# Optimization experiments

Hardware: AMD Instinct MI355X
Metric: run time of the kernel (lower is better)

Reference implementation:

```python
import jax, jax.numpy as jnp
import numpy as np

N, E, IN, HID, H, OUT, G = 20000, 320000, 128, 64, 6, 10, 64
NEG_SLOPE = 0.2


def gat_conv(x, W, a_src, a_dst, b, src, dst):
    # x: [N, F_in]; W: [F_in, H*C]; a_src/a_dst: [H, C]; b: [H*C]
    n = x.shape[0]
    h = (x @ W).reshape(n, H, HID)                      # [N, H, C]
    alpha_s = jnp.einsum('nhc,hc->nh', h, a_src)        # [N, H]
    alpha_d = jnp.einsum('nhc,hc->nh', h, a_dst)
    e = jax.nn.leaky_relu(alpha_s[src] + alpha_d[dst], NEG_SLOPE)  # [E, H]
    # segment softmax over incoming edges of each destination node
    m = jax.ops.segment_max(e, dst, num_segments=n)
    ex = jnp.exp(e - m[dst])
    s = jax.ops.segment_sum(ex, dst, num_segments=n)
    alpha = ex / (s[dst] + 1e-16)                       # [E, H]
    out = jax.ops.segment_sum(alpha[:, :, None] * h[src], dst, num_segments=n)
    return out.reshape(n, H * HID) + b


def setup_inputs() -> dict:
    key = jax.random.key(0)
    ks = jax.random.split(key, 24)
    p = lambda k, shp: jax.random.normal(k, shp, dtype=jnp.float32) * 0.1
    inp = {
        'x': jax.random.normal(ks[0], (N, IN), dtype=jnp.float32),
        'edge_index': jax.random.randint(ks[1], (2, E), 0, N),
        'batch': jnp.sort(jax.random.randint(ks[2], (N,), 0, G)),
        'W1': p(ks[3], (IN, H * HID)), 'a1_src': p(ks[4], (H, HID)), 'a1_dst': p(ks[5], (H, HID)), 'b1': p(ks[6], (H * HID,)),
        'W2': p(ks[7], (H * HID, H * HID)), 'a2_src': p(ks[8], (H, HID)), 'a2_dst': p(ks[9], (H, HID)), 'b2': p(ks[10], (H * HID,)),
        'Ws1': p(ks[11], (IN, H * HID)), 'as1_src': p(ks[12], (H, HID)), 'as1_dst': p(ks[13], (H, HID)), 'bs1': p(ks[14], (H * HID,)),
        'Ws2': p(ks[15], (H * HID, H * HID)), 'as2_src': p(ks[16], (H, HID)), 'as2_dst': p(ks[17], (H, HID)), 'bs2': p(ks[18], (H * HID,)),
        'r1_w': p(ks[19], (H * HID, HID)), 'r1_b': p(ks[20], (HID,)),
        'r2_w': p(ks[21], (HID, OUT)), 'r2_b': p(ks[22], (OUT,)),
    }
    return inp


def reference(x, edge_index, batch, W1, a1_src, a1_dst, b1, W2, a2_src, a2_dst, b2,
              Ws1, as1_src, as1_dst, bs1, Ws2, as2_src, as2_dst, bs2,
              r1_w, r1_b, r2_w, r2_b):
    # PyG GATConv adds self-loops by default
    loop = jnp.arange(N, dtype=edge_index.dtype)
    src = jnp.concatenate([edge_index[0], loop])
    dst = jnp.concatenate([edge_index[1], loop])

    # skip branch (dropout = identity in eval)
    xs = jax.nn.relu(gat_conv(x, Ws1, as1_src, as1_dst, bs1, src, dst))
    xs = jax.nn.relu(gat_conv(xs, Ws2, as2_src, as2_dst, bs2, src, dst))

    # main branch
    h = jax.nn.relu(gat_conv(x, W1, a1_src, a1_dst, b1, src, dst))
    h = jax.nn.relu(gat_conv(h, W2, a2_src, a2_dst, b2, src, dst))

    h = h + xs

    # global mean pool over graphs
    sums = jax.ops.segment_sum(h, batch, num_segments=G)          # [G, H*C]
    cnts = jax.ops.segment_sum(jnp.ones((N,), h.dtype), batch, num_segments=G)
    x_readout = sums / jnp.maximum(cnts, 1.0)[:, None]

    x_global = jax.nn.relu(x_readout @ r1_w + r1_b) @ r2_w + r2_b  # [G, OUT]
    return (jnp.squeeze(x_global), x_readout)
```

## Files before the change

### kernel.cpp

```cpp
#include <hip/hip_runtime.h>
#include <hip/hip_fp16.h>

#define NN 20000
#define EE 320000
#define ETOT 340000
#define FIN 128
#define NH 6
#define FF 384
#define NOUT 10
#define NG 64
#define NEG 0.2f
#define PCH 32
#define NB ((NN + 255) / 256)

typedef short short8 __attribute__((ext_vector_type(8)));
typedef float f32x4 __attribute__((ext_vector_type(4)));

__device__ __half g_h16[(size_t)NN * FF];
__device__ float g_bufB[(size_t)NN * FF];
__device__ float g_bufC[(size_t)NN * FF];
__device__ unsigned short g_featHi[(size_t)NN * FF];
__device__ unsigned short g_xHi[(size_t)NN * FIN];
__device__ unsigned short g_WtHi[4][FF * FF];
__device__ float g_alS[4][NN * NH];
__device__ float g_alD[4][NN * NH];
__device__ int g_rowptr[NN + 1];
__device__ int g_cnt[NN];
__device__ int g_cur[NN];
__device__ int g_blocksum[NB];
__device__ int g_colsrc[ETOT];
__device__ float g_pool[NG * FF];
__device__ int g_gcnt[NG];

__device__ __forceinline__ unsigned short f2bf(float f) {
  unsigned u = __float_as_uint(f);
  u += 0x7FFFu + ((u >> 16) & 1u);
  return (unsigned short)(u >> 16);
}
__device__ __forceinline__ float bf2f(unsigned short s) {
  return __uint_as_float(((unsigned)s) << 16);
}

__device__ __forceinline__ void gl_lds16(const void* g, void* l) {
  __builtin_amdgcn_global_load_lds(
      (const __attribute__((address_space(1))) unsigned int*)(unsigned long long)g,
      (__attribute__((address_space(3))) unsigned int*)(unsigned int)(unsigned long long)l,
      16, 0, 0);
}

__device__ __forceinline__ void mfma_acc(f32x4& c, short8 a, short8 b) {
  asm("v_mfma_f32_16x16x32_bf16 %0, %1, %2, %0" : "+v"(c) : "v"(a), "v"(b));
}

__device__ __forceinline__ void fmix(float2& acc, unsigned hv, float w) {
  asm("v_fma_mix_f32 %0, %2, %3, %0 op_sel:[0,0,0] op_sel_hi:[1,0,0]\n\t"
      "v_fma_mix_f32 %1, %2, %3, %1 op_sel:[1,0,0] op_sel_hi:[1,0,0]"
      : "+v"(acc.x), "+v"(acc.y)
      : "v"(hv), "v"(w));
}

__global__ __launch_bounds__(256) void k_wprep(const float* __restrict__ W, int K, int widx) {
  int i = blockIdx.x * 256 + threadIdx.x;
  if (i >= K * FF) return;
  int k = i / FF, c = i % FF;
  g_WtHi[widx][c * K + k] = f2bf(W[i]);
}

__global__ __launch_bounds__(256) void k_zero() {
  int i = blockIdx.x * 256 + threadIdx.x;
  if (i < NN) g_cnt[i] = 0;
  if (i < NG * FF) g_pool[i] = 0.f;
  if (i < NG) g_gcnt[i] = 0;
  if (i < 4 * NN * NH) {
    (&g_alS[0][0])[i] = 0.f;
    (&g_alD[0][0])[i] = 0.f;
  }
}

__global__ __launch_bounds__(256) void k_hist(const int* __restrict__ ei) {
  int i = blockIdx.x * 256 + threadIdx.x;
  if (i >= ETOT) return;
  int d = (i < EE) ? ei[EE + i] : (i - EE);
  atomicAdd(&g_cnt[d], 1);
}

__global__ __launch_bounds__(256) void k_scan_blk() {
  int b = blockIdx.x;
  int tid = threadIdx.x;
  int i = b * 256 + tid;
  int lane = tid & 63, wid = tid >> 6;
  int v = (i < NN) ? g_cnt[i] : 0;
  int s = v;
  #pragma unroll
  for (int off = 1; off < 64; off <<= 1) {
    int t = __shfl_up(s, off);
    if (lane >= off) s += t;
  }
  __shared__ int wsum[4];
  if (lane == 63) wsum[wid] = s;
  __syncthreads();
  int woff = 0;
  #pragma unroll
  for (int w = 0; w < 4; ++w) woff += (w < wid) ? wsum[w] : 0;
  if (i < NN) g_rowptr[i] = woff + s - v;
  if (tid == 0) g_blocksum[b] = wsum[0] + wsum[1] + wsum[2] + wsum[3];
}

__global__ __launch_bounds__(128) void k_scan_top() {
  int tid = threadIdx.x;
  int lane = tid & 63, wid = tid >> 6;
  int v = (tid < NB) ? g_blocksum[tid] : 0;
  int s = v;
  #pragma unroll
  for (int off = 1; off < 64; off <<= 1) {
    int t = __shfl_up(s, off);
    if (lane >= off) s += t;
  }
  __shared__ int wsum[2];
  if (lane == 63) wsum[wid] = s;
  __syncthreads();
  int woff = (wid == 1) ? wsum[0] : 0;
  int excl = woff + s - v;
  if (tid < NB) g_blocksum[tid] = excl;
  if (tid == NB - 1) g_rowptr[NN] = excl + v;
}

__global__ __launch_bounds__(256) void k_scan_add() {
  int i = blockIdx.x * 256 + threadIdx.x;
  if (i >= NN) return;
  int r = g_rowptr[i] + g_blocksum[blockIdx.x];
  g_rowptr[i] = r;
  g_cur[i] = r;
}

__global__ __launch_bounds__(256) void k_scatter(const int* __restrict__ ei) {
  int i = blockIdx.x * 256 + threadIdx.x;
  if (i >= ETOT) return;
  int s, d;
  if (i < EE) { s = ei[i]; d = ei[EE + i]; } else { s = d = i - EE; }
  int pos = atomicAdd(&g_cur[d], 1);
  g_colsrc[pos] = s;
}

__global__ __launch_bounds__(256) void k_split(const float* __restrict__ xin) {
  int n4 = (NN * FIN) >> 2;
  const float4* s4 = (const float4*)xin;
  ushort4* oh4 = (ushort4*)g_xHi;
  for (int i = blockIdx.x * blockDim.x + threadIdx.x; i < n4; i += gridDim.x * blockDim.x) {
    float4 v = s4[i];
    ushort4 h;
    h.x = f2bf(v.x);
    h.y = f2bf(v.y);
    h.z = f2bf(v.z);
    h.w = f2bf(v.w);
    oh4[i] = h;
  }
}

__global__ __launch_bounds__(256) void k_gemm(int asel, int widx, int K, int layer,
                                              const float* __restrict__ asr,
                                              const float* __restrict__ adt) {
  __shared__ unsigned short lA[128 * 64];
  __shared__ unsigned short lB[128 * 64];
  const unsigned short* Ah = asel ? g_featHi : g_xHi;
  const unsigned short* Bh = g_WtHi[widx];
  const int m0 = blockIdx.x * 128;
  const int n0 = blockIdx.y * 128;
  const int tid = threadIdx.x;
  const int wave = tid >> 6, lane = tid & 63;
  const int wm = wave >> 1, wn = wave & 1;
  const int srow = lane >> 3;
  const int scol = (lane & 7) * 8;

  f32x4 acc[4][4] = {};

  for (int k0 = 0; k0 < K; k0 += 64) {
    __syncthreads();
    #pragma unroll
    for (int it = 0; it < 4; ++it) {
      int c = wave * 4 + it;
      int rA = c * 8 + srow;
      int gr = m0 + rA; gr = (gr < NN) ? gr : (NN - 1);
      gl_lds16(Ah + (size_t)gr * K + k0 + scol, (unsigned short*)lA + c * 512);
      int cB = n0 + rA;
      gl_lds16(Bh + (size_t)cB * K + k0 + scol, (unsigned short*)lB + c * 512);
    }
    __syncthreads();
    #pragma unroll
    for (int kk = 0; kk < 64; kk += 32) {
      const int kb = kk + (lane >> 4) * 8;
      const int r16 = lane & 15;
      short8 af[4], bfr[4];
      #pragma unroll
      for (int mf = 0; mf < 4; ++mf)
        af[mf] = *(const short8*)&lA[(wm * 64 + mf * 16 + r16) * 64 + kb];
      #pragma unroll
      for (int nf = 0; nf < 4; ++nf)
        bfr[nf] = *(const short8*)&lB[(wn * 64 + nf * 16 + r16) * 64 + kb];
      #pragma unroll
      for (int mf = 0; mf < 4; ++mf)
        #pragma unroll
        for (int nf = 0; nf < 4; ++nf)
          mfma_acc(acc[mf][nf], af[mf], bfr[nf]);
    }
  }
  asm volatile("s_nop 7\n\ts_nop 7" :::);

  const int r16 = lane & 15;
  #pragma unroll
  for (int mf = 0; mf < 4; ++mf) {
    #pragma unroll
    for (int nf = 0; nf < 4; ++nf) {
      int col = n0 + wn * 64 + nf * 16 + r16;
      int rb = m0 + wm * 64 + mf * 16 + ((lane >> 4) << 2);
      #pragma unroll
      for (int j = 0; j < 4; ++j) {
        int r = rb + j;
        if (r < NN) g_h16[(size_t)r * FF + col] = __float2half(acc[mf][nf][j]);
      }
    }
  }
  const int hd = blockIdx.y * 2 + wn;
  float as_v[4], ad_v[4];
  #pragma unroll
  for (int nf = 0; nf < 4; ++nf) {
    as_v[nf] = asr[hd * 64 + nf * 16 + r16];
    ad_v[nf] = adt[hd * 64 + nf * 16 + r16];
  }
  float* alS = g_alS[layer];
  float* alD = g_alD[layer];
  #pragma unroll
  for (int mf = 0; mf < 4; ++mf) {
    #pragma unroll
    for (int j = 0; j < 4; ++j) {
      float ps = 0.f, pd = 0.f;
      #pragma unroll
      for (int nf = 0; nf < 4; ++nf) {
        ps = fmaf(acc[mf][nf][j], as_v[nf], ps);
        pd = fmaf(acc[mf][nf][j], ad_v[nf], pd);
      }
      #pragma unroll
      for (int off = 1; off < 16; off <<= 1) {
        ps += __shfl_xor(ps, off);
        pd += __shfl_xor(pd, off);
      }
      int r = m0 + wm * 64 + mf * 16 + ((lane >> 4) << 2) + j;
      if (r16 == 0 && r < NN) {
        atomicAdd(&alS[r * NH + hd], ps);
        atomicAdd(&alD[r * NH + hd], pd);
      }
    }
  }
}

__global__ __launch_bounds__(256) void k_edge(const float* __restrict__ bias, int mode, int layer) {
  int node = blockIdx.x * 4 + (threadIdx.x >> 6);
  int lane = threadIdx.x & 63;
  if (node >= NN) return;
  const float* aS = g_alS[layer];
  const float* aD = g_alD[layer];
  const int lo = g_rowptr[node], hi = g_rowptr[node + 1];
  const int deg = hi - lo;
  float ad[NH];
  #pragma unroll
  for (int h = 0; h < NH; ++h) ad[h] = aD[node * NH + h];

  const bool hiHalf = (lane >= 32);
  int s = 0;
  unsigned wpu[3];
  float m[NH], inv[NH];
  const bool fast = (deg <= 64);

  auto wsel = [&](int u) -> float {
    __half2 hp = *(__half2*)&u;
    return hiHalf ? __high2float(hp) : __low2float(hp);
  };

  if (fast) {
    bool val = lane < deg;
    s = val ? g_colsrc[lo + lane] : 0;
    const float2* ap = (const float2*)(aS + (size_t)s * NH);
    float2 p0 = ap[0], p1 = ap[1], p2 = ap[2];
    float v[NH] = {p0.x + ad[0], p0.y + ad[1], p1.x + ad[2],
                   p1.y + ad[3], p2.x + ad[4], p2.y + ad[5]};
    float mm[NH], w[NH], ss[NH];
    #pragma unroll
    for (int h = 0; h < NH; ++h) {
      v[h] = (v[h] > 0.f) ? v[h] : NEG * v[h];
      mm[h] = val ? v[h] : -1e30f;
    }
    #pragma unroll
    for (int h = 0; h < NH; ++h)
      #pragma unroll
      for (int off = 32; off > 0; off >>= 1)
        mm[h] = fmaxf(mm[h], __shfl_xor(mm[h], off));
    #pragma unroll
    for (int h = 0; h < NH; ++h) {
      w[h] = val ? __expf(v[h] - mm[h]) : 0.f;
      ss[h] = w[h];
    }
    #pragma unroll
    for (int h = 0; h < NH; ++h)
      #pragma unroll
      for (int off = 32; off > 0; off >>= 1)
        ss[h] += __shfl_xor(ss[h], off);
    #pragma unroll
    for (int h = 0; h < NH; ++h) w[h] *= __frcp_rn(ss[h] + 1e-16f);
    __half2 hp0 = __floats2half2_rn(w[0], w[1]);
    __half2 hp1 = __floats2half2_rn(w[2], w[3]);
    __half2 hp2 = __floats2half2_rn(w[4], w[5]);
    wpu[0] = *(unsigned*)&hp0; wpu[1] = *(unsigned*)&hp1; wpu[2] = *(unsigned*)&hp2;
  } else {
    #pragma unroll
    for (int h = 0; h < NH; ++h) m[h] = -1e30f;
    for (int e = lo + lane; e < hi; e += 64) {
      int se = g_colsrc[e];
      #pragma unroll
      for (int h = 0; h < NH; ++h) {
        float v = aS[se * NH + h] + ad[h];
        v = (v > 0.f) ? v : NEG * v;
        m[h] = fmaxf(m[h], v);
      }
    }
    #pragma unroll
    for (int h = 0; h < NH; ++h)
      #pragma unroll
      for (int off = 32; off > 0; off >>= 1)
        m[h] = fmaxf(m[h], __shfl_xor(m[h], off));
    float ss[NH] = {0.f, 0.f, 0.f, 0.f, 0.f, 0.f};
    for (int e = lo + lane; e < hi; e += 64) {
      int se = g_colsrc[e];
      #pragma unroll
      for (int h = 0; h < NH; ++h) {
        float v = aS[se * NH + h] + ad[h];
        v = (v > 0.f) ? v : NEG * v;
        ss[h] += __expf(v - m[h]);
      }
    }
    #pragma unroll
    for (int h = 0; h < NH; ++h) {
      #pragma unroll
      for (int off = 32; off > 0; off >>= 1)
        ss[h] += __shfl_xor(ss[h], off);
      inv[h] = __frcp_rn(ss[h] + 1e-16f);
    }
  }

  float2 accA[3] = {{0.f,0.f},{0.f,0.f},{0.f,0.f}};
  float2 accB[3] = {{0.f,0.f},{0.f,0.f},{0.f,0.f}};
  float2 accC[3] = {{0.f,0.f},{0.f,0.f},{0.f,0.f}};
  float2 accD[3] = {{0.f,0.f},{0.f,0.f},{0.f,0.f}};

  if (fast) {
    int e = 0;
    for (; e + 3 < deg; e += 4) {
      int se0 = __shfl(s, e + 0), se1 = __shfl(s, e + 1);
      int se2 = __shfl(s, e + 2), se3 = __shfl(s, e + 3);
      const unsigned* r0 = (const unsigned*)(g_h16 + (size_t)se0 * FF) + lane;
      const unsigned* r1 = (const unsigned*)(g_h16 + (size_t)se1 * FF) + lane;
      const unsigned* r2 = (const unsigned*)(g_h16 + (size_t)se2 * FF) + lane;
      const unsigned* r3 = (const unsigned*)(g_h16 + (size_t)se3 * FF) + lane;
      unsigned ha[3] = {r0[0], r0[64], r0[128]};
      unsigned hb[3] = {r1[0], r1[64], r1[128]};
      unsigned hc[3] = {r2[0], r2[64], r2[128]};
      unsigned hd[3] = {r3[0], r3[64], r3[128]};
      #pragma unroll
      for (int c = 0; c < 3; ++c) {
        fmix(accA[c], ha[c], wsel(__shfl((int)wpu[c], e + 0)));
        fmix(accB[c], hb[c], wsel(__shfl((int)wpu[c], e + 1)));
        fmix(accC[c], hc[c], wsel(__shfl((int)wpu[c], e + 2)));
        fmix(accD[c], hd[c], wsel(__shfl((int)wpu[c], e + 3)));
      }
    }
    for (; e < deg; ++e) {
      int se = __shfl(s, e);
      const unsigned* r0 = (const unsigned*)(g_h16 + (size_t)se * FF) + lane;
      unsigned h0[3] = {r0[0], r0[64], r0[128]};
      #pragma unroll
      for (int c = 0; c < 3; ++c)
        fmix(accA[c], h0[c], wsel(__shfl((int)wpu[c], e)));
    }
  } else {
    for (int e = 0; e < deg; ++e) {
      int se = g_colsrc[lo + e];
      const float* as = aS + (size_t)se * NH;
      float we[NH];
      #pragma unroll
      for (int h = 0; h < NH; ++h) {
        float v = as[h] + ad[h];
        v = (v > 0.f) ? v : NEG * v;
        we[h] = __expf(v - m[h]) * inv[h];
      }
      float wa[3] = {hiHalf ? we[1] : we[0], hiHalf ? we[3] : we[2],
                     hiHalf ? we[5] : we[4]};
      const unsigned* r0 = (const unsigned*)(g_h16 + (size_t)se * FF) + lane;
      unsigned h0v[3] = {r0[0], r0[64], r0[128]};
      #pragma unroll
      for (int c = 0; c < 3; ++c) fmix(accA[c], h0v[c], wa[c]);
    }
  }

  #pragma unroll
  for (int c = 0; c < 3; ++c) {
    float2 bv = *(const float2*)(bias + c * 128 + lane * 2);
    float ox = fmaxf(accA[c].x + accB[c].x + accC[c].x + accD[c].x + bv.x, 0.f);
    float oy = fmaxf(accA[c].y + accB[c].y + accC[c].y + accD[c].y + bv.y, 0.f);
    size_t off = (size_t)node * FF + c * 128 + lane * 2;
    if (mode == 2) {
      ushort2 hh2 = {f2bf(ox), f2bf(oy)};
      *(ushort2*)(g_featHi + off) = hh2;
    } else {
      float* out = mode ? g_bufC : g_bufB;
      float2 o = {ox, oy};
      *(float2*)(out + off) = o;
    }
  }
}

__global__ __launch_bounds__(384) void k_pool_acc(const int* __restrict__ batch) {
  int n0 = blockIdx.x * PCH;
  if (n0 >= NN) return;
  int n1 = n0 + PCH; if (n1 > NN) n1 = NN;
  int d = threadIdx.x;
  int cur = batch[n0];
  float acc = 0.f;
  int cnt = 0;
  for (int n = n0; n < n1; ++n) {
    int g = batch[n];
    if (g != cur) {
      atomicAdd(&g_pool[cur * FF + d], acc);
      if (d == 0) atomicAdd(&g_gcnt[cur], cnt);
      acc = 0.f; cnt = 0; cur = g;
    }
    acc += g_bufB[(size_t)n * FF + d] + g_bufC[(size_t)n * FF + d];
    ++cnt;
  }
  atomicAdd(&g_pool[cur * FF + d], acc);
  if (d == 0) atomicAdd(&g_gcnt[cur], cnt);
}

__global__ __launch_bounds__(384) void k_finish(const float* __restrict__ r1w,
                                                const float* __restrict__ r1b,
                                                const float* __restrict__ r2w,
                                                const float* __restrict__ r2b,
                                                float* __restrict__ dout) {
  int g = blockIdx.x;
  int d = threadIdx.x;
  __shared__ float xr[FF];
  __shared__ float hid[64];
  int cnt = g_gcnt[g];
  float denom = (cnt > 0) ? (float)cnt : 1.f;
  float v = g_pool[g * FF + d] / denom;
  xr[d] = v;
  dout[NG * NOUT + g * FF + d] = v;
  __syncthreads();
  if (d < 64) {
    float acc = r1b[d];
    for (int k = 0; k < FF; ++k) acc = fmaf(xr[k], r1w[k * 64 + d], acc);
    hid[d] = fmaxf(acc, 0.f);
  }
  __syncthreads();
  if (d < NOUT) {
    float o = r2b[d];
    #pragma unroll
    for (int j = 0; j < 64; ++j) o = fmaf(hid[j], r2w[j * NOUT + d], o);
    dout[g * NOUT + d] = o;
  }
}

extern "C" void kernel_launch(void* const* d_in, const int* in_sizes, int n_in,
                              void* d_out, int out_size, void* d_ws, size_t ws_size,
                              hipStream_t stream) {
  const float* x    = (const float*)d_in[0];
  const int* ei     = (const int*)d_in[1];
  const int* batch  = (const int*)d_in[2];
  const float* W1   = (const float*)d_in[3];
  const float* a1s  = (const float*)d_in[4];
  const float* a1d  = (const float*)d_in[5];
  const float* b1   = (const float*)d_in[6];
  const float* W2   = (const float*)d_in[7];
  const float* a2s  = (const float*)d_in[8];
  const float* a2d  = (const float*)d_in[9];
  const float* b2   = (const float*)d_in[10];
  const float* Ws1  = (const float*)d_in[11];
  const float* as1s = (const float*)d_in[12];
  const float* as1d = (const float*)d_in[13];
  const float* bs1  = (const float*)d_in[14];
  const float* Ws2  = (const float*)d_in[15];
  const float* as2s = (const float*)d_in[16];
  const float* as2d = (const float*)d_in[17];
  const float* bs2  = (const float*)d_in[18];
  const float* r1w  = (const float*)d_in[19];
  const float* r1b  = (const float*)d_in[20];
  const float* r2w  = (const float*)d_in[21];
  const float* r2b  = (const float*)d_in[22];
  float* out = (float*)d_out;

  dim3 b256(256);
  k_wprep<<<dim3((FIN * FF + 255) / 256), b256, 0, stream>>>(Ws1, FIN, 0);
  k_wprep<<<dim3((FF * FF + 255) / 256), b256, 0, stream>>>(Ws2, FF, 1);
  k_wprep<<<dim3((FIN * FF + 255) / 256), b256, 0, stream>>>(W1, FIN, 2);
  k_wprep<<<dim3((FF * FF + 255) / 256), b256, 0, stream>>>(W2, FF, 3);
  k_zero<<<dim3((4 * NN * NH + 255) / 256), b256, 0, stream>>>();
  k_hist<<<dim3((ETOT + 255) / 256), b256, 0, stream>>>(ei);
  k_scan_blk<<<dim3(NB), b256, 0, stream>>>();
  k_scan_top<<<dim3(1), dim3(128), 0, stream>>>();
  k_scan_add<<<dim3(NB), b256, 0, stream>>>();
  k_scatter<<<dim3((ETOT + 255) / 256), b256, 0, stream>>>(ei);
  k_split<<<dim3(2048), b256, 0, stream>>>(x);

  dim3 gemmGrid((NN + 127) / 128, FF / 128);
  dim3 nodeGrid((NN + 3) / 4);

  k_gemm<<<gemmGrid, b256, 0, stream>>>(0, 0, FIN, 0, as1s, as1d);
  k_edge<<<nodeGrid, b256, 0, stream>>>(bs1, 2, 0);
  k_gemm<<<gemmGrid, b256, 0, stream>>>(1, 1, FF, 1, as2s, as2d);
  k_edge<<<nodeGrid, b256, 0, stream>>>(bs2, 1, 1);
  k_gemm<<<gemmGrid, b256, 0, stream>>>(0, 2, FIN, 2, a1s, a1d);
  k_edge<<<nodeGrid, b256, 0, stream>>>(b1, 2, 2);
  k_gemm<<<gemmGrid, b256, 0, stream>>>(1, 3, FF, 3, a2s, a2d);
  k_edge<<<nodeGrid, b256, 0, stream>>>(b2, 0, 3);
  k_pool_acc<<<dim3((NN + PCH - 1) / PCH), dim3(384), 0, stream>>>(batch);
  k_finish<<<dim3(NG), dim3(384), 0, stream>>>(r1w, r1b, r2w, r2b, out);
}
```

Baseline: 358.3 us.

## Batch skip and main GAT branches into single kernel launches per level

The skip and main branches are independent, so each GEMM and edge-aggregation level now runs both branches in one launch using a third grid dimension for the GEMM and a second dimension for the edge kernel. Per-branch feature and projection buffers are duplicated so the two branches can run concurrently. The goal is to cut launch count from eight to four and to fill the GPU better with twice as many blocks per launch. In exchange it uses more memory for the doubled intermediates and may lose some cache locality, since two projection tables are now gathered at the same time.

```diff
diff --git a/kernel.cpp b/kernel.cpp
--- a/kernel.cpp
+++ b/kernel.cpp
@@ -12,14 +12,15 @@
 #define NEG 0.2f
 #define PCH 32
 #define NB ((NN + 255) / 256)
+#define NBLK ((NN + 3) / 4)
 
 typedef short short8 __attribute__((ext_vector_type(8)));
 typedef float f32x4 __attribute__((ext_vector_type(4)));
 
-__device__ __half g_h16[(size_t)NN * FF];
+__device__ __half g_h16[2][(size_t)NN * FF];
+__device__ unsigned short g_feat[2][(size_t)NN * FF];
 __device__ float g_bufB[(size_t)NN * FF];
 __device__ float g_bufC[(size_t)NN * FF];
-__device__ unsigned short g_featHi[(size_t)NN * FF];
 __device__ unsigned short g_xHi[(size_t)NN * FIN];
 __device__ unsigned short g_WtHi[4][FF * FF];
 __device__ float g_alS[4][NN * NH];
@@ -157,13 +158,22 @@
   }
 }
 
-__global__ __launch_bounds__(256) void k_gemm(int asel, int widx, int K, int layer,
-                                              const float* __restrict__ asr,
-                                              const float* __restrict__ adt) {
+__global__ __launch_bounds__(256) void k_gemm(int lvl,
+                                              const float* __restrict__ asr0,
+                                              const float* __restrict__ adt0,
+                                              const float* __restrict__ asr1,
+                                              const float* __restrict__ adt1) {
   __shared__ unsigned short lA[128 * 64];
   __shared__ unsigned short lB[128 * 64];
-  const unsigned short* Ah = asel ? g_featHi : g_xHi;
+  const int br = blockIdx.z;
+  const int layer = (lvl ? 1 : 0) + (br ? 2 : 0);
+  const int widx = layer;
+  const int K = lvl ? FF : FIN;
+  const unsigned short* Ah = lvl ? g_feat[br] : g_xHi;
   const unsigned short* Bh = g_WtHi[widx];
+  const float* asr = br ? asr1 : asr0;
+  const float* adt = br ? adt1 : adt0;
+  __half* hout = g_h16[br];
   const int m0 = blockIdx.x * 128;
   const int n0 = blockIdx.y * 128;
   const int tid = threadIdx.x;
@@ -216,7 +226,7 @@
       #pragma unroll
       for (int j = 0; j < 4; ++j) {
         int r = rb + j;
-        if (r < NN) g_h16[(size_t)r * FF + col] = __float2half(acc[mf][nf][j]);
+        if (r < NN) hout[(size_t)r * FF + col] = __float2half(acc[mf][nf][j]);
       }
     }
   }
@@ -253,10 +263,16 @@
   }
 }
 
-__global__ __launch_bounds__(256) void k_edge(const float* __restrict__ bias, int mode, int layer) {
+__global__ __launch_bounds__(256) void k_edge(int lvl,
+                                              const float* __restrict__ bias0,
+                                              const float* __restrict__ bias1) {
   int node = blockIdx.x * 4 + (threadIdx.x >> 6);
   int lane = threadIdx.x & 63;
   if (node >= NN) return;
+  const int br = blockIdx.y;
+  const int layer = (lvl ? 1 : 0) + (br ? 2 : 0);
+  const float* bias = br ? bias1 : bias0;
+  const __half* htab = g_h16[br];
   const float* aS = g_alS[layer];
   const float* aD = g_alD[layer];
   const int lo = g_rowptr[node], hi = g_rowptr[node + 1];
@@ -356,10 +372,10 @@
     for (; e + 3 < deg; e += 4) {
       int se0 = __shfl(s, e + 0), se1 = __shfl(s, e + 1);
       int se2 = __shfl(s, e + 2), se3 = __shfl(s, e + 3);
-      const unsigned* r0 = (const unsigned*)(g_h16 + (size_t)se0 * FF) + lane;
-      const unsigned* r1 = (const unsigned*)(g_h16 + (size_t)se1 * FF) + lane;
-      const unsigned* r2 = (const unsigned*)(g_h16 + (size_t)se2 * FF) + lane;
-      const unsigned* r3 = (const unsigned*)(g_h16 + (size_t)se3 * FF) + lane;
+      const unsigned* r0 = (const unsigned*)(htab + (size_t)se0 * FF) + lane;
+      const unsigned* r1 = (const unsigned*)(htab + (size_t)se1 * FF) + lane;
+      const unsigned* r2 = (const unsigned*)(htab + (size_t)se2 * FF) + lane;
+      const unsigned* r3 = (const unsigned*)(htab + (size_t)se3 * FF) + lane;
       unsigned ha[3] = {r0[0], r0[64], r0[128]};
       unsigned hb[3] = {r1[0], r1[64], r1[128]};
       unsigned hc[3] = {r2[0], r2[64], r2[128]};
@@ -374,7 +390,7 @@
     }
     for (; e < deg; ++e) {
       int se = __shfl(s, e);
-      const unsigned* r0 = (const unsigned*)(g_h16 + (size_t)se * FF) + lane;
+      const unsigned* r0 = (const unsigned*)(htab + (size_t)se * FF) + lane;
       unsigned h0[3] = {r0[0], r0[64], r0[128]};
       #pragma unroll
       for (int c = 0; c < 3; ++c)
@@ -393,7 +409,7 @@
       }
       float wa[3] = {hiHalf ? we[1] : we[0], hiHalf ? we[3] : we[2],
                      hiHalf ? we[5] : we[4]};
-      const unsigned* r0 = (const unsigned*)(g_h16 + (size_t)se * FF) + lane;
+      const unsigned* r0 = (const unsigned*)(htab + (size_t)se * FF) + lane;
       unsigned h0v[3] = {r0[0], r0[64], r0[128]};
       #pragma unroll
       for (int c = 0; c < 3; ++c) fmix(accA[c], h0v[c], wa[c]);
@@ -406,11 +422,11 @@
     float ox = fmaxf(accA[c].x + accB[c].x + accC[c].x + accD[c].x + bv.x, 0.f);
     float oy = fmaxf(accA[c].y + accB[c].y + accC[c].y + accD[c].y + bv.y, 0.f);
     size_t off = (size_t)node * FF + c * 128 + lane * 2;
-    if (mode == 2) {
+    if (lvl == 0) {
       ushort2 hh2 = {f2bf(ox), f2bf(oy)};
-      *(ushort2*)(g_featHi + off) = hh2;
+      *(ushort2*)(g_feat[br] + off) = hh2;
     } else {
-      float* out = mode ? g_bufC : g_bufB;
+      float* out = br ? g_bufB : g_bufC;
       float2 o = {ox, oy};
       *(float2*)(out + off) = o;
     }
@@ -509,17 +525,13 @@
   k_scatter<<<dim3((ETOT + 255) / 256), b256, 0, stream>>>(ei);
   k_split<<<dim3(2048), b256, 0, stream>>>(x);
 
-  dim3 gemmGrid((NN + 127) / 128, FF / 128);
-  dim3 nodeGrid((NN + 3) / 4);
-
-  k_gemm<<<gemmGrid, b256, 0, stream>>>(0, 0, FIN, 0, as1s, as1d);
-  k_edge<<<nodeGrid, b256, 0, stream>>>(bs1, 2, 0);
-  k_gemm<<<gemmGrid, b256, 0, stream>>>(1, 1, FF, 1, as2s, as2d);
-  k_edge<<<nodeGrid, b256, 0, stream>>>(bs2, 1, 1);
-  k_gemm<<<gemmGrid, b256, 0, stream>>>(0, 2, FIN, 2, a1s, a1d);
-  k_edge<<<nodeGrid, b256, 0, stream>>>(b1, 2, 2);
-  k_gemm<<<gemmGrid, b256, 0, stream>>>(1, 3, FF, 3, a2s, a2d);
-  k_edge<<<nodeGrid, b256, 0, stream>>>(b2, 0, 3);
+  dim3 gemmGrid((NN + 127) / 128, FF / 128, 2);
+  dim3 edgeGrid(NBLK, 2);
+
+  k_gemm<<<gemmGrid, b256, 0, stream>>>(0, as1s, as1d, a1s, a1d);
+  k_edge<<<edgeGrid, b256, 0, stream>>>(0, bs1, b1);
+  k_gemm<<<gemmGrid, b256, 0, stream>>>(1, as2s, as2d, a2s, a2d);
+  k_edge<<<edgeGrid, b256, 0, stream>>>(1, bs2, b2);
   k_pool_acc<<<dim3((NN + PCH - 1) / PCH), dim3(384), 0, stream>>>(batch);
   k_finish<<<dim3(NG), dim3(384), 0, stream>>>(r1w, r1b, r2w, r2b, out);
 }
```

Result: faster. 327.8 us (-8.5%).
